# Performance work log

Hardware: AMD Instinct MI355X
Metric: run time of the kernel (lower is better)

Reference implementation:

```python
import jax, jax.numpy as jnp
import numpy as np

B, N, D, OUT = 8, 2048, 128, 128

def setup_inputs() -> dict:
    key = jax.random.key(0)
    k1, k2, k3, k4 = jax.random.split(key, 4)
    input_ = jax.random.normal(k1, (B, N, D), dtype=jnp.float32)
    adj_matrix = jax.random.randint(k2, (B, N, N), 0, 2, dtype=jnp.int32)
    W = jax.random.normal(k3, (2 * D, OUT), dtype=jnp.float32) * 0.05
    b = jax.random.normal(k4, (OUT,), dtype=jnp.float32) * 0.05
    return {"input_": input_, "adj_matrix": adj_matrix, "W": W, "b": b}

def reference(input_, adj_matrix, W, b):
    adj = adj_matrix.astype(jnp.float32)           # [B,N,N]
    deg = jnp.sum(adj, axis=2)                     # [B,N]
    deg = jnp.where(deg == 0, 1.0, deg)
    agg = jnp.einsum('bnm,bmd->bnd', adj, input_) / deg[:, :, None]  # mean aggregation
    feat = jnp.concatenate([input_, agg], axis=2)  # [B,N,2D]
    out = jax.nn.sigmoid(feat @ W + b)             # [B,N,OUT]
    out = out / jnp.linalg.norm(out, axis=2, keepdims=True)
    return out
```

## Files before the change

kernel.cpp:

```cpp
#include <hip/hip_runtime.h>

#define Bn 8
#define Nn 2048
#define Dn 128
#define OUTn 128

typedef __attribute__((ext_vector_type(8))) short bf16x8;
typedef __attribute__((ext_vector_type(8))) unsigned short ushort8;
typedef __attribute__((ext_vector_type(4))) float f32x4;
typedef __attribute__((ext_vector_type(4))) int int4v;
typedef __attribute__((ext_vector_type(4))) unsigned int uint4v;
typedef __attribute__((ext_vector_type(4))) float float4v;

__device__ __forceinline__ unsigned short f2bf(float f) {
  unsigned int u = __builtin_bit_cast(unsigned int, f);
  u += 0x7FFFu + ((u >> 16) & 1u);
  return (unsigned short)(u >> 16);
}

__global__ __launch_bounds__(256) void gcn_prep(const float* __restrict__ in,
                                                const float* __restrict__ W,
                                                unsigned short* __restrict__ inT,
                                                unsigned short* __restrict__ WT) {
  const int tid = threadIdx.x;
  if (blockIdx.x >= 256) {
    int gid = (blockIdx.x - 256) * 256 + tid;
    int j = gid >> 8, k = gid & 255;
    WT[gid] = f2bf(W[k * OUTn + j]);
    return;
  }
  const int b = blockIdx.x >> 5;
  const int n0 = (blockIdx.x & 31) * 64;
  __shared__ __attribute__((aligned(16))) unsigned short lds[64][130];
  #pragma unroll
  for (int c = 0; c < 32; ++c) {
    int e = tid + c * 256;
    int i = e >> 7, d = e & 127;
    lds[i][d] = f2bf(in[((size_t)(b * Nn + n0 + i)) * Dn + d]);
  }
  __syncthreads();
  #pragma unroll
  for (int c = 0; c < 4; ++c) {
    int ch = tid + c * 256;
    int d = ch >> 3, g = (ch & 7) * 8;
    ushort8 v;
    #pragma unroll
    for (int e = 0; e < 8; ++e) v[e] = lds[g + e][d];
    *(ushort8*)(inT + ((size_t)(b * Dn + d)) * Nn + n0 + g) = v;
  }
}

union SMem {
  struct {
    int A[3][64][64];
    unsigned short Bs[3][128][64];
  } s;
  struct {
    unsigned short aggl[64][136];
    float rowsum[64][2];
    float degs[64];
  } e;
};

#define STAGE(cur, kt) do {                                                    \
    _Pragma("unroll")                                                          \
    for (int c_ = 0; c_ < 2; ++c_) {                                           \
      const int r_ = wv * 8 + c_ * 4 + (l >> 4);                               \
      const int cg_ = (l & 15) ^ (r_ & 7);                                     \
      const int* gsrc_ = adjB + (size_t)r_ * Nn + (kt) * 64 + cg_ * 4;         \
      __builtin_amdgcn_global_load_lds(                                        \
          (const __attribute__((address_space(1))) void*)gsrc_,                \
          (__attribute__((address_space(3))) void*)(smc + (cur) * 16384 +      \
                                                   wv * 2048 + c_ * 1024),     \
          16, 0, 0);                                                           \
    }                                                                          \
    _Pragma("unroll")                                                          \
    for (int c_ = 0; c_ < 2; ++c_) {                                           \
      const int d_ = wv * 16 + c_ * 8 + (l >> 3);                              \
      const int cg_ = (l & 7) ^ (d_ & 7);                                      \
      const unsigned short* gsrc_ = inTb + (size_t)d_ * Nn + (kt) * 64 + cg_ * 8; \
      __builtin_amdgcn_global_load_lds(                                        \
          (const __attribute__((address_space(1))) void*)gsrc_,                \
          (__attribute__((address_space(3))) void*)(smc + 49152 +              \
                                                   (cur) * 16384 +             \
                                                   wv * 2048 + c_ * 1024),     \
          16, 0, 0);                                                           \
    }                                                                          \
  } while (0)

#define COMPUTE(cur) do {                                                      \
    const char* Abase = smc + (cur) * 16384 + (rg * 16 + lr) * 256;            \
    const char* Bbase = smc + 49152 + (cur) * 16384;                           \
    _Pragma("unroll")                                                          \
    for (int kc = 0; kc < 2; ++kc) {                                           \
      const int c0_ = kc * 8 + lg * 2;                                         \
      int4v ai0 = *(const int4v*)(Abase + ((c0_ ^ swz8) * 16));                \
      int4v ai1 = *(const int4v*)(Abase + (((c0_ + 1) ^ swz8) * 16));          \
      dsum += ai0[0] + ai0[1] + ai0[2] + ai0[3] +                              \
              ai1[0] + ai1[1] + ai1[2] + ai1[3];                               \
      uint4v aw;                                                               \
      aw[0] = (unsigned)ai0[0] * 0x3F80u + (unsigned)ai0[1] * 0x3F800000u;     \
      aw[1] = (unsigned)ai0[2] * 0x3F80u + (unsigned)ai0[3] * 0x3F800000u;     \
      aw[2] = (unsigned)ai1[0] * 0x3F80u + (unsigned)ai1[1] * 0x3F800000u;     \
      aw[3] = (unsigned)ai1[2] * 0x3F80u + (unsigned)ai1[3] * 0x3F800000u;     \
      bf16x8 af = __builtin_bit_cast(bf16x8, aw);                              \
      _Pragma("unroll")                                                        \
      for (int cf = 0; cf < 4; ++cf) {                                         \
        const int brow_ = ch * 64 + cf * 16 + lr;                              \
        bf16x8 bfm = *(const bf16x8*)(Bbase + (size_t)brow_ * 128 +            \
                                      (((kc * 4 + lg) ^ swz8) * 16));          \
        acc[cf] = __builtin_amdgcn_mfma_f32_16x16x32_bf16(af, bfm, acc[cf],    \
                                                          0, 0, 0);            \
      }                                                                        \
    }                                                                          \
  } while (0)

#define WAITBAR(N) do {                                                        \
    asm volatile("s_waitcnt vmcnt(" #N ")" ::: "memory");                      \
    __builtin_amdgcn_s_barrier();                                              \
    __builtin_amdgcn_sched_barrier(0);                                         \
  } while (0)

__global__ __launch_bounds__(512, 2) void gcn_main(
    const float* __restrict__ input_, const int* __restrict__ adj,
    const float* __restrict__ bvec, const unsigned short* __restrict__ inT,
    const unsigned short* __restrict__ WT, float* __restrict__ out) {
  __shared__ SMem sm;
  char* smc = (char*)&sm;
  const int tid = threadIdx.x;
  const int wv = tid >> 6;
  const int l = tid & 63, lr = l & 15, lg = (l >> 4) & 3;
  const int rg = wv >> 1, ch = wv & 1;

  const int swz = (blockIdx.x & 7) * 32 + (blockIdx.x >> 3);
  const int bb = swz >> 5;
  const int row0 = (swz & 31) * 64;
  const int grow0 = bb * Nn + row0;

  const int* adjB = adj + (size_t)grow0 * Nn;
  const unsigned short* inTb = inT + (size_t)bb * Dn * Nn;

  const int swz8 = lr & 7;
  f32x4 acc[4] = {};
  int dsum = 0;

  STAGE(0, 0);
  STAGE(1, 1);

  #pragma unroll 1
  for (int j = 0; j < 10; ++j) {
    const int kt = 3 * j;
    WAITBAR(4); STAGE(2, kt + 2); COMPUTE(0);
    WAITBAR(4); STAGE(0, kt + 3); COMPUTE(1);
    WAITBAR(4); STAGE(1, kt + 4); COMPUTE(2);
  }
  WAITBAR(4); COMPUTE(0);
  WAITBAR(0); COMPUTE(1);

  __syncthreads();

  {
    int s = dsum;
    s += __shfl_xor(s, 16);
    s += __shfl_xor(s, 32);
    if (l < 16) sm.e.degs[rg * 16 + l] = (s == 0) ? 1.0f : (float)s;
  }
  __syncthreads();

  float dgi[4];
  #pragma unroll
  for (int reg = 0; reg < 4; ++reg)
    dgi[reg] = 1.0f / sm.e.degs[rg * 16 + lg * 4 + reg];
  #pragma unroll
  for (int cf = 0; cf < 4; ++cf)
    #pragma unroll
    for (int reg = 0; reg < 4; ++reg)
      sm.e.aggl[rg * 16 + lg * 4 + reg][ch * 64 + cf * 16 + lr] =
          f2bf(acc[cf][reg] * dgi[reg]);
  __syncthreads();

  f32x4 acc2[4] = {};
  const float* xrow = input_ + (size_t)(grow0 + rg * 16 + lr) * Dn;
  #pragma unroll
  for (int ks = 0; ks < 8; ++ks) {
    bf16x8 af;
    if (ks < 4) {
      float4v f0 = *(const float4v*)(xrow + ks * 32 + lg * 8);
      float4v f1 = *(const float4v*)(xrow + ks * 32 + lg * 8 + 4);
      ushort8 vv;
      #pragma unroll
      for (int e = 0; e < 4; ++e) { vv[e] = f2bf(f0[e]); vv[e + 4] = f2bf(f1[e]); }
      af = __builtin_bit_cast(bf16x8, vv);
    } else {
      af = *(const bf16x8*)&sm.e.aggl[rg * 16 + lr][(ks - 4) * 32 + lg * 8];
    }
    #pragma unroll
    for (int cf = 0; cf < 4; ++cf) {
      bf16x8 bw = *(const bf16x8*)(WT + (size_t)(ch * 64 + cf * 16 + lr) * 256 +
                                   ks * 32 + lg * 8);
      acc2[cf] = __builtin_amdgcn_mfma_f32_16x16x32_bf16(af, bw, acc2[cf], 0, 0, 0);
    }
  }

  float bcol[4];
  #pragma unroll
  for (int cf = 0; cf < 4; ++cf) bcol[cf] = bvec[ch * 64 + cf * 16 + lr];
  float sg[4][4];
  #pragma unroll
  for (int cf = 0; cf < 4; ++cf)
    #pragma unroll
    for (int reg = 0; reg < 4; ++reg) {
      float x = acc2[cf][reg] + bcol[cf];
      sg[cf][reg] = 1.0f / (1.0f + expf(-x));
    }
  #pragma unroll
  for (int reg = 0; reg < 4; ++reg) {
    float p = 0.f;
    #pragma unroll
    for (int cf = 0; cf < 4; ++cf) p += sg[cf][reg] * sg[cf][reg];
    p += __shfl_xor(p, 1);
    p += __shfl_xor(p, 2);
    p += __shfl_xor(p, 4);
    p += __shfl_xor(p, 8);
    if (lr == 0) sm.e.rowsum[rg * 16 + lg * 4 + reg][ch] = p;
  }
  __syncthreads();
  #pragma unroll
  for (int reg = 0; reg < 4; ++reg) {
    const int row = rg * 16 + lg * 4 + reg;
    float nrm = rsqrtf(sm.e.rowsum[row][0] + sm.e.rowsum[row][1]);
    #pragma unroll
    for (int cf = 0; cf < 4; ++cf)
      out[(size_t)(grow0 + row) * OUTn + ch * 64 + cf * 16 + lr] =
          sg[cf][reg] * nrm;
  }
}

extern "C" void kernel_launch(void* const* d_in, const int* in_sizes, int n_in,
                              void* d_out, int out_size, void* d_ws, size_t ws_size,
                              hipStream_t stream) {
  (void)in_sizes; (void)n_in; (void)out_size; (void)ws_size;
  const float* input_ = (const float*)d_in[0];
  const int* adj = (const int*)d_in[1];
  const float* W = (const float*)d_in[2];
  const float* bvec = (const float*)d_in[3];
  float* out = (float*)d_out;

  unsigned short* inT = (unsigned short*)d_ws;
  unsigned short* WT = inT + (size_t)Bn * Dn * Nn;

  hipLaunchKernelGGL(gcn_prep, dim3(384), dim3(256), 0, stream, input_, W, inT, WT);
  hipLaunchKernelGGL(gcn_main, dim3(256), dim3(512), 0, stream,
                     input_, adj, bvec, inT, WT, out);
}
```

Before: 42.53 us.

## Load adjacency tiles directly into registers instead of staging through LDS

```diff
diff --git a/kernel.cpp b/kernel.cpp
--- a/kernel.cpp
+++ b/kernel.cpp
@@ -51,10 +51,7 @@
 }
 
 union SMem {
-  struct {
-    int A[3][64][64];
-    unsigned short Bs[3][128][64];
-  } s;
+  unsigned short Bs[3][128][64];
   struct {
     unsigned short aggl[64][136];
     float rowsum[64][2];
@@ -62,18 +59,12 @@
   } e;
 };
 
-#define STAGE(cur, kt) do {                                                    \
-    _Pragma("unroll")                                                          \
-    for (int c_ = 0; c_ < 2; ++c_) {                                           \
-      const int r_ = wv * 8 + c_ * 4 + (l >> 4);                               \
-      const int cg_ = (l & 15) ^ (r_ & 7);                                     \
-      const int* gsrc_ = adjB + (size_t)r_ * Nn + (kt) * 64 + cg_ * 4;         \
-      __builtin_amdgcn_global_load_lds(                                        \
-          (const __attribute__((address_space(1))) void*)gsrc_,                \
-          (__attribute__((address_space(3))) void*)(smc + (cur) * 16384 +      \
-                                                   wv * 2048 + c_ * 1024),     \
-          16, 0, 0);                                                           \
-    }                                                                          \
+#define STAGE(ab, cur, kt) do {                                                \
+    ab[0] = *(const int4v*)(pA);                                               \
+    ab[1] = *(const int4v*)(pA + 4);                                           \
+    ab[2] = *(const int4v*)(pA + 32);                                          \
+    ab[3] = *(const int4v*)(pA + 36);                                          \
+    pA += 64;                                \
     _Pragma("unroll")                                                          \
     for (int c_ = 0; c_ < 2; ++c_) {                                           \
       const int d_ = wv * 16 + c_ * 8 + (l >> 3);                              \
@@ -81,21 +72,18 @@
       const unsigned short* gsrc_ = inTb + (size_t)d_ * Nn + (kt) * 64 + cg_ * 8; \
       __builtin_amdgcn_global_load_lds(                                        \
           (const __attribute__((address_space(1))) void*)gsrc_,                \
-          (__attribute__((address_space(3))) void*)(smc + 49152 +              \
-                                                   (cur) * 16384 +             \
+          (__attribute__((address_space(3))) void*)(smc + (cur) * 16384 +      \
                                                    wv * 2048 + c_ * 1024),     \
           16, 0, 0);                                                           \
     }                                                                          \
   } while (0)
 
-#define COMPUTE(cur) do {                                                      \
-    const char* Abase = smc + (cur) * 16384 + (rg * 16 + lr) * 256;            \
-    const char* Bbase = smc + 49152 + (cur) * 16384;                           \
+#define COMPUTE(ab, cur) do {                                                  \
+    const char* Bbase = smc + (cur) * 16384;                                   \
     _Pragma("unroll")                                                          \
     for (int kc = 0; kc < 2; ++kc) {                                           \
-      const int c0_ = kc * 8 + lg * 2;                                         \
-      int4v ai0 = *(const int4v*)(Abase + ((c0_ ^ swz8) * 16));                \
-      int4v ai1 = *(const int4v*)(Abase + (((c0_ + 1) ^ swz8) * 16));          \
+      int4v ai0 = ab[kc * 2];                                                  \
+      int4v ai1 = ab[kc * 2 + 1];                                              \
       dsum += ai0[0] + ai0[1] + ai0[2] + ai0[3] +                              \
               ai1[0] + ai1[1] + ai1[2] + ai1[3];                               \
       uint4v aw;                                                               \
@@ -137,25 +125,28 @@
   const int row0 = (swz & 31) * 64;
   const int grow0 = bb * Nn + row0;
 
-  const int* adjB = adj + (size_t)grow0 * Nn;
   const unsigned short* inTb = inT + (size_t)bb * Dn * Nn;
+
+  const int* pA = adj + (size_t)(grow0 + rg * 16 + lr) * Nn + lg * 8;
 
   const int swz8 = lr & 7;
   f32x4 acc[4] = {};
   int dsum = 0;
 
-  STAGE(0, 0);
-  STAGE(1, 1);
+  int4v aT0[4], aT1[4], aT2[4];
+
+  STAGE(aT0, 0, 0);
+  STAGE(aT1, 1, 1);
 
   #pragma unroll 1
   for (int j = 0; j < 10; ++j) {
     const int kt = 3 * j;
-    WAITBAR(4); STAGE(2, kt + 2); COMPUTE(0);
-    WAITBAR(4); STAGE(0, kt + 3); COMPUTE(1);
-    WAITBAR(4); STAGE(1, kt + 4); COMPUTE(2);
-  }
-  WAITBAR(4); COMPUTE(0);
-  WAITBAR(0); COMPUTE(1);
+    WAITBAR(6); STAGE(aT2, 2, kt + 2); COMPUTE(aT0, 0);
+    WAITBAR(6); STAGE(aT0, 0, kt + 3); COMPUTE(aT1, 1);
+    WAITBAR(6); STAGE(aT1, 1, kt + 4); COMPUTE(aT2, 2);
+  }
+  WAITBAR(6); COMPUTE(aT0, 0);
+  WAITBAR(0); COMPUTE(aT1, 1);
 
   __syncthreads();
 
```

After: 62.39 us. 46.7% more time.

## Bit-pack adjacency and compute degrees in prep kernel, consume bitmask in main

Applied to the files above, without the earlier changes.

```diff
diff --git a/kernel.cpp b/kernel.cpp
--- a/kernel.cpp
+++ b/kernel.cpp
@@ -8,8 +8,6 @@
 typedef __attribute__((ext_vector_type(8))) short bf16x8;
 typedef __attribute__((ext_vector_type(8))) unsigned short ushort8;
 typedef __attribute__((ext_vector_type(4))) float f32x4;
-typedef __attribute__((ext_vector_type(4))) int int4v;
-typedef __attribute__((ext_vector_type(4))) unsigned int uint4v;
 typedef __attribute__((ext_vector_type(4))) float float4v;
 
 __device__ __forceinline__ unsigned short f2bf(float f) {
@@ -18,62 +16,72 @@
   return (unsigned short)(u >> 16);
 }
 
-__global__ __launch_bounds__(256) void gcn_prep(const float* __restrict__ in,
-                                                const float* __restrict__ W,
-                                                unsigned short* __restrict__ inT,
-                                                unsigned short* __restrict__ WT) {
+__global__ __launch_bounds__(256) void gcn_prep(
+    const float* __restrict__ in, const int* __restrict__ adj,
+    const float* __restrict__ W, unsigned long long* __restrict__ adjP,
+    float* __restrict__ deg, unsigned short* __restrict__ inT,
+    unsigned short* __restrict__ WT) {
+  __shared__ __attribute__((aligned(16))) unsigned short lds[64][130];
   const int tid = threadIdx.x;
-  if (blockIdx.x >= 256) {
-    int gid = (blockIdx.x - 256) * 256 + tid;
-    int j = gid >> 8, k = gid & 255;
-    WT[gid] = f2bf(W[k * OUTn + j]);
+  const int bid = blockIdx.x;
+
+  if (bid < 4096) {
+    const int wv = tid >> 6, l = tid & 63;
+    const int row = bid * 4 + wv;
+    const int* rp = adj + (size_t)row * Nn;
+    int v[32];
+    #pragma unroll
+    for (int k = 0; k < 32; ++k) v[k] = rp[k * 64 + l];
+    unsigned long long myw = 0;
+    int cnt = 0;
+    #pragma unroll
+    for (int k = 0; k < 32; ++k) {
+      unsigned long long w = __ballot(v[k] != 0);
+      cnt += __popcll(w);
+      if (l == k) myw = w;
+    }
+    if (l < 32) adjP[(size_t)row * 32 + l] = myw;
+    if (l == 0) deg[row] = (cnt == 0) ? 1.0f : (float)cnt;
     return;
   }
-  const int b = blockIdx.x >> 5;
-  const int n0 = (blockIdx.x & 31) * 64;
-  __shared__ __attribute__((aligned(16))) unsigned short lds[64][130];
-  #pragma unroll
-  for (int c = 0; c < 32; ++c) {
-    int e = tid + c * 256;
-    int i = e >> 7, d = e & 127;
-    lds[i][d] = f2bf(in[((size_t)(b * Nn + n0 + i)) * Dn + d]);
-  }
-  __syncthreads();
-  #pragma unroll
-  for (int c = 0; c < 4; ++c) {
-    int ch = tid + c * 256;
-    int d = ch >> 3, g = (ch & 7) * 8;
-    ushort8 v;
-    #pragma unroll
-    for (int e = 0; e < 8; ++e) v[e] = lds[g + e][d];
-    *(ushort8*)(inT + ((size_t)(b * Dn + d)) * Nn + n0 + g) = v;
-  }
+  if (bid < 4352) {
+    const int b = (bid - 4096) >> 5;
+    const int n0 = ((bid - 4096) & 31) * 64;
+    #pragma unroll
+    for (int c = 0; c < 32; ++c) {
+      int e = tid + c * 256;
+      int i = e >> 7, d = e & 127;
+      lds[i][d] = f2bf(in[((size_t)(b * Nn + n0 + i)) * Dn + d]);
+    }
+    __syncthreads();
+    #pragma unroll
+    for (int c = 0; c < 4; ++c) {
+      int ch = tid + c * 256;
+      int d = ch >> 3, g = (ch & 7) * 8;
+      ushort8 vv;
+      #pragma unroll
+      for (int e = 0; e < 8; ++e) vv[e] = lds[g + e][d];
+      *(ushort8*)(inT + ((size_t)(b * Dn + d)) * Nn + n0 + g) = vv;
+    }
+    return;
+  }
+  int gid = (bid - 4352) * 256 + tid;
+  int j = gid >> 8, k = gid & 255;
+  WT[gid] = f2bf(W[k * OUTn + j]);
 }
 
 union SMem {
   struct {
-    int A[3][64][64];
+    unsigned long long A[64][33];
     unsigned short Bs[3][128][64];
   } s;
   struct {
     unsigned short aggl[64][136];
     float rowsum[64][2];
-    float degs[64];
   } e;
 };
 
 #define STAGE(cur, kt) do {                                                    \
-    _Pragma("unroll")                                                          \
-    for (int c_ = 0; c_ < 2; ++c_) {                                           \
-      const int r_ = wv * 8 + c_ * 4 + (l >> 4);                               \
-      const int cg_ = (l & 15) ^ (r_ & 7);                                     \
-      const int* gsrc_ = adjB + (size_t)r_ * Nn + (kt) * 64 + cg_ * 4;         \
-      __builtin_amdgcn_global_load_lds(                                        \
-          (const __attribute__((address_space(1))) void*)gsrc_,                \
-          (__attribute__((address_space(3))) void*)(smc + (cur) * 16384 +      \
-                                                   wv * 2048 + c_ * 1024),     \
-          16, 0, 0);                                                           \
-    }                                                                          \
     _Pragma("unroll")                                                          \
     for (int c_ = 0; c_ < 2; ++c_) {                                           \
       const int d_ = wv * 16 + c_ * 8 + (l >> 3);                              \
@@ -81,29 +89,25 @@
       const unsigned short* gsrc_ = inTb + (size_t)d_ * Nn + (kt) * 64 + cg_ * 8; \
       __builtin_amdgcn_global_load_lds(                                        \
           (const __attribute__((address_space(1))) void*)gsrc_,                \
-          (__attribute__((address_space(3))) void*)(smc + 49152 +              \
+          (__attribute__((address_space(3))) void*)(smc + 16896 +              \
                                                    (cur) * 16384 +             \
                                                    wv * 2048 + c_ * 1024),     \
           16, 0, 0);                                                           \
     }                                                                          \
   } while (0)
 
-#define COMPUTE(cur) do {                                                      \
-    const char* Abase = smc + (cur) * 16384 + (rg * 16 + lr) * 256;            \
-    const char* Bbase = smc + 49152 + (cur) * 16384;                           \
+#define COMPUTE(cur, kt) do {                                                  \
+    const char* Bbase = smc + 16896 + (cur) * 16384;                           \
+    const unsigned long long aw_ = sm.s.A[rg * 16 + lr][kt];                   \
     _Pragma("unroll")                                                          \
     for (int kc = 0; kc < 2; ++kc) {                                           \
-      const int c0_ = kc * 8 + lg * 2;                                         \
-      int4v ai0 = *(const int4v*)(Abase + ((c0_ ^ swz8) * 16));                \
-      int4v ai1 = *(const int4v*)(Abase + (((c0_ + 1) ^ swz8) * 16));          \
-      dsum += ai0[0] + ai0[1] + ai0[2] + ai0[3] +                              \
-              ai1[0] + ai1[1] + ai1[2] + ai1[3];                               \
-      uint4v aw;                                                               \
-      aw[0] = (unsigned)ai0[0] * 0x3F80u + (unsigned)ai0[1] * 0x3F800000u;     \
-      aw[1] = (unsigned)ai0[2] * 0x3F80u + (unsigned)ai0[3] * 0x3F800000u;     \
-      aw[2] = (unsigned)ai1[0] * 0x3F80u + (unsigned)ai1[1] * 0x3F800000u;     \
-      aw[3] = (unsigned)ai1[2] * 0x3F80u + (unsigned)ai1[3] * 0x3F800000u;     \
-      bf16x8 af = __builtin_bit_cast(bf16x8, aw);                              \
+      unsigned int bits = (unsigned int)(aw_ >> (kc * 32 + lg * 8)) & 0xFFu;   \
+      ushort8 av;                                                              \
+      _Pragma("unroll")                                                        \
+      for (int e = 0; e < 8; ++e)                                              \
+        av[e] = (bits & (1u << e)) ? (unsigned short)0x3F80u                   \
+                                   : (unsigned short)0u;                       \
+      bf16x8 af = __builtin_bit_cast(bf16x8, av);                              \
       _Pragma("unroll")                                                        \
       for (int cf = 0; cf < 4; ++cf) {                                         \
         const int brow_ = ch * 64 + cf * 16 + lr;                              \
@@ -122,9 +126,10 @@
   } while (0)
 
 __global__ __launch_bounds__(512, 2) void gcn_main(
-    const float* __restrict__ input_, const int* __restrict__ adj,
-    const float* __restrict__ bvec, const unsigned short* __restrict__ inT,
-    const unsigned short* __restrict__ WT, float* __restrict__ out) {
+    const float* __restrict__ input_, const unsigned long long* __restrict__ adjP,
+    const float* __restrict__ deg, const float* __restrict__ bvec,
+    const unsigned short* __restrict__ inT, const unsigned short* __restrict__ WT,
+    float* __restrict__ out) {
   __shared__ SMem sm;
   char* smc = (char*)&sm;
   const int tid = threadIdx.x;
@@ -137,12 +142,19 @@
   const int row0 = (swz & 31) * 64;
   const int grow0 = bb * Nn + row0;
 
-  const int* adjB = adj + (size_t)grow0 * Nn;
   const unsigned short* inTb = inT + (size_t)bb * Dn * Nn;
-
   const int swz8 = lr & 7;
   f32x4 acc[4] = {};
-  int dsum = 0;
+
+  {
+    const unsigned long long* src = adjP + (size_t)grow0 * 32 + tid * 4;
+    #pragma unroll
+    for (int j = 0; j < 4; ++j) {
+      int idx = tid * 4 + j;
+      sm.s.A[idx >> 5][idx & 31] = src[j];
+    }
+  }
+  __syncthreads();
 
   STAGE(0, 0);
   STAGE(1, 1);
@@ -150,27 +162,19 @@
   #pragma unroll 1
   for (int j = 0; j < 10; ++j) {
     const int kt = 3 * j;
-    WAITBAR(4); STAGE(2, kt + 2); COMPUTE(0);
-    WAITBAR(4); STAGE(0, kt + 3); COMPUTE(1);
-    WAITBAR(4); STAGE(1, kt + 4); COMPUTE(2);
-  }
-  WAITBAR(4); COMPUTE(0);
-  WAITBAR(0); COMPUTE(1);
-
-  __syncthreads();
-
-  {
-    int s = dsum;
-    s += __shfl_xor(s, 16);
-    s += __shfl_xor(s, 32);
-    if (l < 16) sm.e.degs[rg * 16 + l] = (s == 0) ? 1.0f : (float)s;
-  }
+    WAITBAR(2); STAGE(2, kt + 2); COMPUTE(0, kt);
+    WAITBAR(2); STAGE(0, kt + 3); COMPUTE(1, kt + 1);
+    WAITBAR(2); STAGE(1, kt + 4); COMPUTE(2, kt + 2);
+  }
+  WAITBAR(2); COMPUTE(0, 30);
+  WAITBAR(0); COMPUTE(1, 31);
+
   __syncthreads();
 
   float dgi[4];
   #pragma unroll
   for (int reg = 0; reg < 4; ++reg)
-    dgi[reg] = 1.0f / sm.e.degs[rg * 16 + lg * 4 + reg];
+    dgi[reg] = 1.0f / deg[grow0 + rg * 16 + lg * 4 + reg];
   #pragma unroll
   for (int cf = 0; cf < 4; ++cf)
     #pragma unroll
@@ -248,8 +252,12 @@
 
   unsigned short* inT = (unsigned short*)d_ws;
   unsigned short* WT = inT + (size_t)Bn * Dn * Nn;
-
-  hipLaunchKernelGGL(gcn_prep, dim3(384), dim3(256), 0, stream, input_, W, inT, WT);
+  unsigned long long* adjP =
+      (unsigned long long*)((char*)d_ws + 4194304 + 65536);
+  float* deg = (float*)((char*)d_ws + 4194304 + 65536 + 4194304);
+
+  hipLaunchKernelGGL(gcn_prep, dim3(4480), dim3(256), 0, stream,
+                     input_, adj, W, adjP, deg, inT, WT);
   hipLaunchKernelGGL(gcn_main, dim3(256), dim3(512), 0, stream,
-                     input_, adj, bvec, inT, WT, out);
-}
+                     input_, adjP, deg, bvec, inT, WT, out);
+}
```

Measured after the change: 56.96 us. 33.9% more time.
